# Optimization experiments

Hardware: AMD Instinct MI355X
Metric: run time of the kernel (lower is better)

## Reference

```python
import jax, jax.numpy as jnp
import numpy as np

B, R, F, H, DIM = 256, 64, 2048, 512, 512

def setup_inputs() -> dict:
    key = jax.random.key(0)
    ks = jax.random.split(key, 8)
    s = lambda n: 1.0 / np.sqrt(n)
    return {
        "features": jax.random.normal(ks[0], (B, R, F), jnp.float32),
        "prev": jax.random.normal(ks[1], (B, H), jnp.float32),
        "W_w": jax.random.normal(ks[2], (F, DIM), jnp.float32) * s(F),
        "W_b": jnp.zeros((DIM,), jnp.float32),
        "W2_w": jax.random.normal(ks[3], (H, DIM), jnp.float32) * s(H),
        "W2_b": jnp.zeros((DIM,), jnp.float32),
        "W3_w": jax.random.normal(ks[4], (DIM, 1), jnp.float32) * s(DIM),
        "W3_b": jnp.zeros((1,), jnp.float32),
    }

def reference(features, prev, W_w, W_b, W2_w, W2_b, W3_w, W3_b):
    # prev: [B,H] -> [B,1,DIM]
    p = (prev @ W2_w + W2_b)[:, None, :]
    # features: [B,R,F] -> [B,R,DIM]
    c = jnp.einsum('brf,fd->brd', features, W_w) + W_b
    c = jnp.tanh(c + p)
    score = jnp.einsum('brd,do->bro', c, W3_w) + W3_b  # [B,R,1]
    aw = jax.nn.softmax(score, axis=1)
    q = jnp.sum(aw * features, axis=1)  # [B,F]
    return q
```

## Files before the change

kernel.cpp:

```cpp
#include <hip/hip_runtime.h>
#include <hip/hip_bf16.h>


#define B_ 256
#define R_ 64
#define F_ 2048
#define H_ 512
#define DIM_ 512

typedef short bf16x8 __attribute__((ext_vector_type(8)));
typedef float f32x4 __attribute__((ext_vector_type(4)));

__device__ __forceinline__ ushort f2bf(float x) {
  __hip_bfloat16 h = __float2bfloat16(x);
  return __builtin_bit_cast(ushort, h);
}

__device__ __forceinline__ uint4 pack8(float4 x, float4 y) {
  uint4 r;
  r.x = (uint)f2bf(x.x) | ((uint)f2bf(x.y) << 16);
  r.y = (uint)f2bf(x.z) | ((uint)f2bf(x.w) << 16);
  r.z = (uint)f2bf(y.x) | ((uint)f2bf(y.y) << 16);
  r.w = (uint)f2bf(y.z) | ((uint)f2bf(y.w) << 16);
  return r;
}

__device__ __forceinline__ void gld16(const float* g, float* l) {
  __builtin_amdgcn_global_load_lds(
      (const __attribute__((address_space(1))) unsigned int*)(g),
      (__attribute__((address_space(3))) unsigned int*)(l),
      16, 0, 0);
}

__global__ void pack_w_k(const float* __restrict__ Ww, ushort* __restrict__ wpack) {
  int idx = blockIdx.x * 256 + threadIdx.x;
  float v = Ww[idx];
  int k = idx >> 9;
  int d = idx & 511;
  int kt = k >> 5, kr = k & 31;
  int g = kr >> 3, i = kr & 7;
  int ctg = d >> 4, c = d & 15;
  size_t dst = ((size_t)((kt * 32 + ctg) * 64 + g * 16 + c)) * 8 + (size_t)i;
  wpack[dst] = f2bf(v);
}

__global__ __launch_bounds__(256) void prep_p_k(const float* __restrict__ prev,
                                                const float* __restrict__ W2w,
                                                const float* __restrict__ W2b,
                                                const float* __restrict__ Wb,
                                                float* __restrict__ pprime) {
  __shared__ float lprev[8][H_];
  int bg = blockIdx.x >> 3;
  int d0 = (blockIdx.x & 7) * 64;
  int t = threadIdx.x;
  const float4* src = reinterpret_cast<const float4*>(prev + (size_t)bg * 8 * H_);
  float4* dst = reinterpret_cast<float4*>(&lprev[0][0]);
  for (int i = t; i < 8 * H_ / 4; i += 256) dst[i] = src[i];
  __syncthreads();
  int d = d0 + (t & 63);
  int bq = t >> 6;
  float a0 = 0.f, a1 = 0.f;
  #pragma unroll 8
  for (int h = 0; h < H_; ++h) {
    float wv = W2w[h * DIM_ + d];
    a0 += lprev[bq][h] * wv;
    a1 += lprev[bq + 4][h] * wv;
  }
  float bias = W2b[d] + Wb[d];
  pprime[(size_t)(bg * 8 + bq) * DIM_ + d] = a0 + bias;
  pprime[(size_t)(bg * 8 + bq + 4) * DIM_ + d] = a1 + bias;
}

__device__ __forceinline__ float fast_tanh(float x) {
  float e = __expf(2.f * x);
  return 1.f - 2.f / (e + 1.f);
}

__global__ __launch_bounds__(512, 4) void score_k(const float* __restrict__ feat,
                                                  const ushort* __restrict__ wpack,
                                                  const float* __restrict__ pprime,
                                                  const float* __restrict__ W3,
                                                  float* __restrict__ sp) {
  int slice = blockIdx.x >> 8;
  int b = blockIdx.x & 255;
  int t = threadIdx.x;
  int wid = t >> 6;
  int l = t & 63;
  int l15 = l & 15, g = l >> 4;
  const float* featB = feat + (size_t)b * R_ * F_;

  __shared__ float raw[3][4096];
  __shared__ uint4 frg[2][512];
  __shared__ float lds_part[8][R_];

  f32x4 acc[4][2];
  #pragma unroll
  for (int rt = 0; rt < 4; ++rt)
    #pragma unroll
    for (int ct = 0; ct < 2; ++ct)
      acc[rt][ct] = (f32x4){0.f, 0.f, 0.f, 0.f};

  int srow = wid * 4 + g;
  int sch = l15 ^ (srow & 15);
  const float* sg0 = featB + (size_t)srow * F_ + sch * 4;
  const float* sg1 = featB + (size_t)(srow + 32) * F_ + sch * 4;

  int crow = t >> 3, cj2 = (t & 7) * 2;
  int rm = crow & 15;
  int cw = (t & 7) * 64 + (crow ^ (cj2 & 15));

  const ushort* wp = wpack + (size_t)(slice * 16 + wid * 2) * 512 + (size_t)l * 8;

#define STAGE(buf, kt) do {                                        \
    gld16(sg0 + (size_t)(kt) * 64, &raw[buf][wid * 256]);          \
    gld16(sg1 + (size_t)(kt) * 64, &raw[buf][2048 + wid * 256]);   \
  } while (0)

#define LOADB(dst, kt) do {                                        \
    const ushort* wpk_ = wp + (size_t)(kt) * 32768;                \
    dst[0][0] = *reinterpret_cast<const uint4*>(wpk_);             \
    dst[0][1] = *reinterpret_cast<const uint4*>(wpk_ + 512);       \
    dst[1][0] = *reinterpret_cast<const uint4*>(wpk_ + 16384);     \
    dst[1][1] = *reinterpret_cast<const uint4*>(wpk_ + 16384 + 512); \
  } while (0)

#define CVT(nb, fb) do {                                           \
    const float* rb_ = &raw[nb][crow * 64];                        \
    float4 x_ = *reinterpret_cast<const float4*>(rb_ + ((cj2 + 0) ^ rm) * 4); \
    float4 y_ = *reinterpret_cast<const float4*>(rb_ + ((cj2 + 1) ^ rm) * 4); \
    frg[fb][cw] = pack8(x_, y_);                                   \
  } while (0)

#define MFMA_STEP(fb) do {                                         \
    _Pragma("unroll")                                              \
    for (int s_ = 0; s_ < 2; ++s_) {                               \
      bf16x8 af_[4];                                               \
      int kc_ = s_ * 4 + g;                                        \
      _Pragma("unroll")                                            \
      for (int rt_ = 0; rt_ < 4; ++rt_)                            \
        af_[rt_] = __builtin_bit_cast(bf16x8,                      \
            frg[fb][kc_ * 64 + ((rt_ * 16 + l15) ^ ((kc_ * 2) & 15))]); \
      _Pragma("unroll")                                            \
      for (int ct_ = 0; ct_ < 2; ++ct_) {                          \
        bf16x8 bv_ = __builtin_bit_cast(bf16x8, bc[s_][ct_]);      \
        _Pragma("unroll")                                          \
        for (int rt_ = 0; rt_ < 4; ++rt_)                          \
          acc[rt_][ct_] = __builtin_amdgcn_mfma_f32_16x16x32_bf16( \
              af_[rt_], bv_, acc[rt_][ct_], 0, 0, 0);              \
      }                                                            \
    }                                                              \
  } while (0)

  uint4 bc[2][2];
  STAGE(0, 0);
  STAGE(1, 1);
  LOADB(bc, 0);
  asm volatile("s_waitcnt vmcnt(6)" ::: "memory");
  __builtin_amdgcn_s_barrier();
  asm volatile("" ::: "memory");
  STAGE(2, 2);
  CVT(0, 0);

  int cur3 = 0;
  for (int kt = 0; kt < 32; ++kt) {
    uint4 bn[2][2];
    if (kt < 31) LOADB(bn, kt + 1);
    if (kt < 30) {
      asm volatile("s_waitcnt vmcnt(10) lgkmcnt(0)" ::: "memory");
    } else if (kt == 30) {
      asm volatile("s_waitcnt vmcnt(8) lgkmcnt(0)" ::: "memory");
    } else {
      asm volatile("s_waitcnt lgkmcnt(0)" ::: "memory");
    }
    __builtin_amdgcn_s_barrier();
    asm volatile("" ::: "memory");

    if (kt < 29) STAGE(cur3, kt + 3);
    int nxt3 = (cur3 == 2) ? 0 : cur3 + 1;
    if (kt < 31) CVT(nxt3, (kt + 1) & 1);
    MFMA_STEP(kt & 1);
    if (kt < 31) {
      #pragma unroll
      for (int s_ = 0; s_ < 2; ++s_)
        #pragma unroll
        for (int ct_ = 0; ct_ < 2; ++ct_)
          bc[s_][ct_] = bn[s_][ct_];
    }
    cur3 = nxt3;
  }

#undef STAGE
#undef LOADB
#undef CVT
#undef MFMA_STEP

  float pp[2], w3v[2];
  #pragma unroll
  for (int ct = 0; ct < 2; ++ct) {
    int col = slice * 256 + wid * 32 + ct * 16 + l15;
    pp[ct] = pprime[b * DIM_ + col];
    w3v[ct] = W3[col];
  }
  #pragma unroll
  for (int rt = 0; rt < 4; ++rt) {
    #pragma unroll
    for (int j = 0; j < 4; ++j) {
      float v = fast_tanh(acc[rt][0][j] + pp[0]) * w3v[0]
              + fast_tanh(acc[rt][1][j] + pp[1]) * w3v[1];
      v += __shfl_xor(v, 1);
      v += __shfl_xor(v, 2);
      v += __shfl_xor(v, 4);
      v += __shfl_xor(v, 8);
      if (l15 == 0) lds_part[wid][rt * 16 + g * 4 + j] = v;
    }
  }
  __syncthreads();

  if (t < R_) {
    float s = 0.f;
    #pragma unroll
    for (int w = 0; w < 8; ++w) s += lds_part[w][t];
    sp[((size_t)b * 2 + slice) * R_ + t] = s;
  }
}

__global__ __launch_bounds__(256) void wsum_k(const float* __restrict__ feat,
                                              const float* __restrict__ sp,
                                              float* __restrict__ out) {
  int b = blockIdx.x >> 2;
  int f0 = (blockIdx.x & 3) * 512;
  int t = threadIdx.x;
  __shared__ float lds_aw[R_];

  if (t < R_) {
    float s = sp[((size_t)b * 2 + 0) * R_ + t] + sp[((size_t)b * 2 + 1) * R_ + t];
    float m = s;
    #pragma unroll
    for (int off = 32; off >= 1; off >>= 1) m = fmaxf(m, __shfl_xor(m, off));
    float e = __expf(s - m);
    float su = e;
    #pragma unroll
    for (int off = 32; off >= 1; off >>= 1) su += __shfl_xor(su, off);
    lds_aw[t] = e / su;
  }
  __syncthreads();

  const float* fp = feat + (size_t)b * R_ * F_ + f0 + t * 2;
  float qx = 0.f, qy = 0.f;
  #pragma unroll 8
  for (int r = 0; r < R_; ++r) {
    float a = lds_aw[r];
    float2 v = *reinterpret_cast<const float2*>(fp + (size_t)r * F_);
    qx += a * v.x;
    qy += a * v.y;
  }
  *reinterpret_cast<float2*>(out + (size_t)b * F_ + f0 + t * 2) = (float2){qx, qy};
}

extern "C" void kernel_launch(void* const* d_in, const int* in_sizes, int n_in,
                              void* d_out, int out_size, void* d_ws, size_t ws_size,
                              hipStream_t stream) {
  const float* feat = (const float*)d_in[0];
  const float* prev = (const float*)d_in[1];
  const float* Ww   = (const float*)d_in[2];
  const float* Wb   = (const float*)d_in[3];
  const float* W2w  = (const float*)d_in[4];
  const float* W2b  = (const float*)d_in[5];
  const float* W3w  = (const float*)d_in[6];
  float* out = (float*)d_out;

  ushort* wpack  = (ushort*)d_ws;
  float*  pprime = (float*)((char*)d_ws + (size_t)F_ * DIM_ * 2);
  float*  sp     = (float*)((char*)d_ws + (size_t)F_ * DIM_ * 2
                                        + (size_t)B_ * DIM_ * 4);

  pack_w_k<<<(F_ * DIM_) / 256, 256, 0, stream>>>(Ww, wpack);
  prep_p_k<<<256, 256, 0, stream>>>(prev, W2w, W2b, Wb, pprime);
  score_k<<<B_ * 2, 512, 0, stream>>>(feat, wpack, pprime, W3w, sp);
  wsum_k<<<B_ * 4, 256, 0, stream>>>(feat, sp, out);
}
```

Measured before the change: 103.4 us.

## Enlarge score GEMM tile to 128x256 with 2x4 wave grid and XCD-aware block swizzle

Each score_k block now computes 128 rows (two batch items) by 256 columns instead of 64x256, with waves arranged 2x4 and each wave holding a 64x64 accumulator tile. The larger tile halves the number of packed-weight reads per feature row and cuts the grid to 256 blocks, remapped so neighbouring logical tiles land on the same XCD. The staging ring drops from three buffers to two, and the MFMA phase is wrapped in s_setprio. In exchange, register pressure and LDS use per block go up, occupancy drops to 2 blocks per CU, and the shallower prefetch pipeline may expose more memory latency.

```diff
diff --git a/kernel.cpp b/kernel.cpp
--- a/kernel.cpp
+++ b/kernel.cpp
@@ -76,117 +76,121 @@
   return 1.f - 2.f / (e + 1.f);
 }
 
-__global__ __launch_bounds__(512, 4) void score_k(const float* __restrict__ feat,
+__global__ __launch_bounds__(512, 2) void score_k(const float* __restrict__ feat,
                                                   const ushort* __restrict__ wpack,
                                                   const float* __restrict__ pprime,
                                                   const float* __restrict__ W3,
                                                   float* __restrict__ sp) {
-  int slice = blockIdx.x >> 8;
-  int b = blockIdx.x & 255;
+  int bid = blockIdx.x;
+  int logical = (bid & 7) * 32 + (bid >> 3);
+  int rowblk = logical >> 1;
+  int colblk = logical & 1;
   int t = threadIdx.x;
   int wid = t >> 6;
-  int l = t & 63;
-  int l15 = l & 15, g = l >> 4;
-  const float* featB = feat + (size_t)b * R_ * F_;
-
-  __shared__ float raw[3][4096];
-  __shared__ uint4 frg[2][512];
+  int wm = wid >> 2, wn = wid & 3;
+  int l = t & 63, l15 = l & 15, g = l >> 4;
+
+  const float* featT = feat + (size_t)rowblk * 128 * F_;
+
+  __shared__ float4 raw4[2][2048];
+  __shared__ uint4 frg[2][1024];
   __shared__ float lds_part[8][R_];
 
-  f32x4 acc[4][2];
+  f32x4 acc[4][4];
   #pragma unroll
   for (int rt = 0; rt < 4; ++rt)
     #pragma unroll
-    for (int ct = 0; ct < 2; ++ct)
+    for (int ct = 0; ct < 4; ++ct)
       acc[rt][ct] = (f32x4){0.f, 0.f, 0.f, 0.f};
 
-  int srow = wid * 4 + g;
-  int sch = l15 ^ (srow & 15);
-  const float* sg0 = featB + (size_t)srow * F_ + sch * 4;
-  const float* sg1 = featB + (size_t)(srow + 32) * F_ + sch * 4;
-
-  int crow = t >> 3, cj2 = (t & 7) * 2;
+  const float* sgj[4];
+  #pragma unroll
+  for (int j = 0; j < 4; ++j) {
+    int r_ = wid * 16 + j * 4 + g;
+    int ch = l15 ^ (r_ & 15);
+    sgj[j] = featT + (size_t)r_ * F_ + ch * 4;
+  }
+
+  int crow = t >> 2;
   int rm = crow & 15;
-  int cw = (t & 7) * 64 + (crow ^ (cj2 & 15));
-
-  const ushort* wp = wpack + (size_t)(slice * 16 + wid * 2) * 512 + (size_t)l * 8;
-
-#define STAGE(buf, kt) do {                                        \
-    gld16(sg0 + (size_t)(kt) * 64, &raw[buf][wid * 256]);          \
-    gld16(sg1 + (size_t)(kt) * 64, &raw[buf][2048 + wid * 256]);   \
-  } while (0)
-
-#define LOADB(dst, kt) do {                                        \
-    const ushort* wpk_ = wp + (size_t)(kt) * 32768;                \
-    dst[0][0] = *reinterpret_cast<const uint4*>(wpk_);             \
-    dst[0][1] = *reinterpret_cast<const uint4*>(wpk_ + 512);       \
-    dst[1][0] = *reinterpret_cast<const uint4*>(wpk_ + 16384);     \
-    dst[1][1] = *reinterpret_cast<const uint4*>(wpk_ + 16384 + 512); \
-  } while (0)
-
-#define CVT(nb, fb) do {                                           \
-    const float* rb_ = &raw[nb][crow * 64];                        \
-    float4 x_ = *reinterpret_cast<const float4*>(rb_ + ((cj2 + 0) ^ rm) * 4); \
-    float4 y_ = *reinterpret_cast<const float4*>(rb_ + ((cj2 + 1) ^ rm) * 4); \
-    frg[fb][cw] = pack8(x_, y_);                                   \
-  } while (0)
-
-#define MFMA_STEP(fb) do {                                         \
-    _Pragma("unroll")                                              \
-    for (int s_ = 0; s_ < 2; ++s_) {                               \
-      bf16x8 af_[4];                                               \
-      int kc_ = s_ * 4 + g;                                        \
-      _Pragma("unroll")                                            \
-      for (int rt_ = 0; rt_ < 4; ++rt_)                            \
-        af_[rt_] = __builtin_bit_cast(bf16x8,                      \
-            frg[fb][kc_ * 64 + ((rt_ * 16 + l15) ^ ((kc_ * 2) & 15))]); \
-      _Pragma("unroll")                                            \
-      for (int ct_ = 0; ct_ < 2; ++ct_) {                          \
-        bf16x8 bv_ = __builtin_bit_cast(bf16x8, bc[s_][ct_]);      \
-        _Pragma("unroll")                                          \
-        for (int rt_ = 0; rt_ < 4; ++rt_)                          \
-          acc[rt_][ct_] = __builtin_amdgcn_mfma_f32_16x16x32_bf16( \
-              af_[rt_], bv_, acc[rt_][ct_], 0, 0, 0);              \
-      }                                                            \
-    }                                                              \
-  } while (0)
-
-  uint4 bc[2][2];
+  int cq = (t & 3) * 2;
+
+  int ctg0 = colblk * 16 + wn * 4;
+
+#define STAGE(buf, kt) do {                                          \
+    _Pragma("unroll")                                                \
+    for (int j_ = 0; j_ < 4; ++j_)                                   \
+      gld16(sgj[j_] + (size_t)(kt) * 64,                             \
+            (float*)&raw4[buf][(wid * 16 + j_ * 4) * 16]);           \
+  } while (0)
+
+#define LOADB(dst, kt) do {                                          \
+    _Pragma("unroll")                                                \
+    for (int s_ = 0; s_ < 2; ++s_)                                   \
+      _Pragma("unroll")                                              \
+      for (int ct_ = 0; ct_ < 4; ++ct_)                              \
+        dst[s_][ct_] = *reinterpret_cast<const uint4*>(              \
+            wpack + ((size_t)((kt) * 2 + s_) * 32 + (ctg0 + ct_)) * 512 + (size_t)l * 8); \
+  } while (0)
+
+#define CVT(rb, fb) do {                                             \
+    _Pragma("unroll")                                                \
+    for (int h_ = 0; h_ < 2; ++h_) {                                 \
+      int kc_ = cq + h_;                                             \
+      float4 x_ = raw4[rb][crow * 16 + ((kc_ * 2) ^ rm)];            \
+      float4 y_ = raw4[rb][crow * 16 + ((kc_ * 2 + 1) ^ rm)];        \
+      frg[fb][kc_ * 128 + crow] = pack8(x_, y_);                     \
+    }                                                                \
+  } while (0)
+
+#define MFMA_STEP(fb) do {                                           \
+    _Pragma("unroll")                                                \
+    for (int s_ = 0; s_ < 2; ++s_) {                                 \
+      bf16x8 af_[4];                                                 \
+      _Pragma("unroll")                                              \
+      for (int rt_ = 0; rt_ < 4; ++rt_)                              \
+        af_[rt_] = __builtin_bit_cast(bf16x8,                        \
+            frg[fb][(s_ * 4 + g) * 128 + wm * 64 + rt_ * 16 + l15]); \
+      _Pragma("unroll")                                              \
+      for (int ct_ = 0; ct_ < 4; ++ct_) {                            \
+        bf16x8 bv_ = __builtin_bit_cast(bf16x8, bc[s_][ct_]);        \
+        _Pragma("unroll")                                            \
+        for (int rt_ = 0; rt_ < 4; ++rt_)                            \
+          acc[rt_][ct_] = __builtin_amdgcn_mfma_f32_16x16x32_bf16(   \
+              af_[rt_], bv_, acc[rt_][ct_], 0, 0, 0);                \
+      }                                                              \
+    }                                                                \
+  } while (0)
+
+  uint4 bc[2][4], bn[2][4];
   STAGE(0, 0);
   STAGE(1, 1);
   LOADB(bc, 0);
-  asm volatile("s_waitcnt vmcnt(6)" ::: "memory");
-  __builtin_amdgcn_s_barrier();
-  asm volatile("" ::: "memory");
-  STAGE(2, 2);
+  asm volatile("s_waitcnt vmcnt(12)" ::: "memory");
   CVT(0, 0);
 
-  int cur3 = 0;
   for (int kt = 0; kt < 32; ++kt) {
-    uint4 bn[2][2];
     if (kt < 31) LOADB(bn, kt + 1);
-    if (kt < 30) {
-      asm volatile("s_waitcnt vmcnt(10) lgkmcnt(0)" ::: "memory");
-    } else if (kt == 30) {
+    if (kt < 31) {
       asm volatile("s_waitcnt vmcnt(8) lgkmcnt(0)" ::: "memory");
     } else {
-      asm volatile("s_waitcnt lgkmcnt(0)" ::: "memory");
+      asm volatile("s_waitcnt vmcnt(0) lgkmcnt(0)" ::: "memory");
     }
     __builtin_amdgcn_s_barrier();
     asm volatile("" ::: "memory");
 
-    if (kt < 29) STAGE(cur3, kt + 3);
-    int nxt3 = (cur3 == 2) ? 0 : cur3 + 1;
-    if (kt < 31) CVT(nxt3, (kt + 1) & 1);
+    if (kt < 30) STAGE(kt & 1, kt + 2);
+    if (kt < 31) CVT((kt + 1) & 1, (kt + 1) & 1);
+    __builtin_amdgcn_s_setprio(1);
     MFMA_STEP(kt & 1);
+    __builtin_amdgcn_s_setprio(0);
     if (kt < 31) {
       #pragma unroll
       for (int s_ = 0; s_ < 2; ++s_)
         #pragma unroll
-        for (int ct_ = 0; ct_ < 2; ++ct_)
+        for (int ct_ = 0; ct_ < 4; ++ct_)
           bc[s_][ct_] = bn[s_][ct_];
     }
-    cur3 = nxt3;
   }
 
 #undef STAGE
@@ -194,11 +198,12 @@
 #undef CVT
 #undef MFMA_STEP
 
-  float pp[2], w3v[2];
-  #pragma unroll
-  for (int ct = 0; ct < 2; ++ct) {
-    int col = slice * 256 + wid * 32 + ct * 16 + l15;
-    pp[ct] = pprime[b * DIM_ + col];
+  int b0 = rowblk * 2;
+  float pp[4], w3v[4];
+  #pragma unroll
+  for (int ct = 0; ct < 4; ++ct) {
+    int col = colblk * 256 + wn * 64 + ct * 16 + l15;
+    pp[ct] = pprime[(b0 + wm) * DIM_ + col];
     w3v[ct] = W3[col];
   }
   #pragma unroll
@@ -206,7 +211,9 @@
     #pragma unroll
     for (int j = 0; j < 4; ++j) {
       float v = fast_tanh(acc[rt][0][j] + pp[0]) * w3v[0]
-              + fast_tanh(acc[rt][1][j] + pp[1]) * w3v[1];
+              + fast_tanh(acc[rt][1][j] + pp[1]) * w3v[1]
+              + fast_tanh(acc[rt][2][j] + pp[2]) * w3v[2]
+              + fast_tanh(acc[rt][3][j] + pp[3]) * w3v[3];
       v += __shfl_xor(v, 1);
       v += __shfl_xor(v, 2);
       v += __shfl_xor(v, 4);
@@ -216,11 +223,12 @@
   }
   __syncthreads();
 
-  if (t < R_) {
-    float s = 0.f;
-    #pragma unroll
-    for (int w = 0; w < 8; ++w) s += lds_part[w][t];
-    sp[((size_t)b * 2 + slice) * R_ + t] = s;
+  if (t < 128) {
+    int bb = t >> 6;
+    int r = t & 63;
+    float s = lds_part[bb * 4 + 0][r] + lds_part[bb * 4 + 1][r]
+            + lds_part[bb * 4 + 2][r] + lds_part[bb * 4 + 3][r];
+    sp[((size_t)(b0 + bb) * 2 + colblk) * R_ + r] = s;
   }
 }
 
@@ -276,6 +284,6 @@
 
   pack_w_k<<<(F_ * DIM_) / 256, 256, 0, stream>>>(Ww, wpack);
   prep_p_k<<<256, 256, 0, stream>>>(prev, W2w, W2b, Wb, pprime);
-  score_k<<<B_ * 2, 512, 0, stream>>>(feat, wpack, pprime, W3w, sp);
+  score_k<<<256, 512, 0, stream>>>(feat, wpack, pprime, W3w, sp);
   wsum_k<<<B_ * 4, 256, 0, stream>>>(feat, sp, out);
 }
```

Result: slower. 113.2 us (+9.5%).

## Merge setup kernels and unroll score k-loop with double B registers and setprio

Applied to the files above, without the earlier changes.

Merges the weight-packing and prev-projection kernels into one launch, with a block-index split, to save one kernel launch. The score kernel's k-loop is unrolled by two and uses two ping-pong B-fragment register sets instead of copying the next fragments each iteration. MFMA sections are wrapped in s_setprio to favour the math waves. The triple-buffer indices are tracked explicitly, and the final iterations are peeled with adjusted waitcnts. Register pressure and code size grow.

```diff
diff --git a/kernel.cpp b/kernel.cpp
--- a/kernel.cpp
+++ b/kernel.cpp
@@ -32,26 +32,29 @@
       16, 0, 0);
 }
 
-__global__ void pack_w_k(const float* __restrict__ Ww, ushort* __restrict__ wpack) {
-  int idx = blockIdx.x * 256 + threadIdx.x;
-  float v = Ww[idx];
-  int k = idx >> 9;
-  int d = idx & 511;
-  int kt = k >> 5, kr = k & 31;
-  int g = kr >> 3, i = kr & 7;
-  int ctg = d >> 4, c = d & 15;
-  size_t dst = ((size_t)((kt * 32 + ctg) * 64 + g * 16 + c)) * 8 + (size_t)i;
-  wpack[dst] = f2bf(v);
-}
-
-__global__ __launch_bounds__(256) void prep_p_k(const float* __restrict__ prev,
-                                                const float* __restrict__ W2w,
-                                                const float* __restrict__ W2b,
-                                                const float* __restrict__ Wb,
-                                                float* __restrict__ pprime) {
+__global__ __launch_bounds__(256) void setup_k(const float* __restrict__ Ww,
+                                               ushort* __restrict__ wpack,
+                                               const float* __restrict__ prev,
+                                               const float* __restrict__ W2w,
+                                               const float* __restrict__ W2b,
+                                               const float* __restrict__ Wb,
+                                               float* __restrict__ pprime) {
   __shared__ float lprev[8][H_];
-  int bg = blockIdx.x >> 3;
-  int d0 = (blockIdx.x & 7) * 64;
+  if (blockIdx.x < 4096) {
+    int idx = blockIdx.x * 256 + threadIdx.x;
+    float v = Ww[idx];
+    int k = idx >> 9;
+    int d = idx & 511;
+    int kt = k >> 5, kr = k & 31;
+    int g = kr >> 3, i = kr & 7;
+    int ctg = d >> 4, c = d & 15;
+    size_t dst = ((size_t)((kt * 32 + ctg) * 64 + g * 16 + c)) * 8 + (size_t)i;
+    wpack[dst] = f2bf(v);
+    return;
+  }
+  int pb = blockIdx.x - 4096;
+  int bg = pb >> 3;
+  int d0 = (pb & 7) * 64;
   int t = threadIdx.x;
   const float4* src = reinterpret_cast<const float4*>(prev + (size_t)bg * 8 * H_);
   float4* dst = reinterpret_cast<float4*>(&lprev[0][0]);
@@ -107,7 +110,7 @@
 
   int crow = t >> 3, cj2 = (t & 7) * 2;
   int rm = crow & 15;
-  int cw = (t & 7) * 64 + (crow ^ (cj2 & 15));
+  int cw = (t & 7) * 64 + (crow ^ cj2);
 
   const ushort* wp = wpack + (size_t)(slice * 16 + wid * 2) * 512 + (size_t)l * 8;
 
@@ -131,7 +134,7 @@
     frg[fb][cw] = pack8(x_, y_);                                   \
   } while (0)
 
-#define MFMA_STEP(fb) do {                                         \
+#define MFMA_STEP(fb, BSET) do {                                   \
     _Pragma("unroll")                                              \
     for (int s_ = 0; s_ < 2; ++s_) {                               \
       bf16x8 af_[4];                                               \
@@ -142,7 +145,7 @@
             frg[fb][kc_ * 64 + ((rt_ * 16 + l15) ^ ((kc_ * 2) & 15))]); \
       _Pragma("unroll")                                            \
       for (int ct_ = 0; ct_ < 2; ++ct_) {                          \
-        bf16x8 bv_ = __builtin_bit_cast(bf16x8, bc[s_][ct_]);      \
+        bf16x8 bv_ = __builtin_bit_cast(bf16x8, BSET[s_][ct_]);    \
         _Pragma("unroll")                                          \
         for (int rt_ = 0; rt_ < 4; ++rt_)                          \
           acc[rt_][ct_] = __builtin_amdgcn_mfma_f32_16x16x32_bf16( \
@@ -151,48 +154,72 @@
     }                                                              \
   } while (0)
 
-  uint4 bc[2][2];
+#define BARRIER_VM(N) do {                                         \
+    asm volatile("s_waitcnt vmcnt(" #N ") lgkmcnt(0)" ::: "memory"); \
+    __builtin_amdgcn_s_barrier();                                  \
+    asm volatile("" ::: "memory");                                 \
+  } while (0)
+
+  uint4 bA[2][2], bB[2][2];
   STAGE(0, 0);
   STAGE(1, 1);
-  LOADB(bc, 0);
+  LOADB(bA, 0);
   asm volatile("s_waitcnt vmcnt(6)" ::: "memory");
   __builtin_amdgcn_s_barrier();
   asm volatile("" ::: "memory");
   STAGE(2, 2);
   CVT(0, 0);
 
-  int cur3 = 0;
-  for (int kt = 0; kt < 32; ++kt) {
-    uint4 bn[2][2];
-    if (kt < 31) LOADB(bn, kt + 1);
-    if (kt < 30) {
-      asm volatile("s_waitcnt vmcnt(10) lgkmcnt(0)" ::: "memory");
-    } else if (kt == 30) {
-      asm volatile("s_waitcnt vmcnt(8) lgkmcnt(0)" ::: "memory");
-    } else {
-      asm volatile("s_waitcnt lgkmcnt(0)" ::: "memory");
-    }
-    __builtin_amdgcn_s_barrier();
-    asm volatile("" ::: "memory");
-
-    if (kt < 29) STAGE(cur3, kt + 3);
-    int nxt3 = (cur3 == 2) ? 0 : cur3 + 1;
-    if (kt < 31) CVT(nxt3, (kt + 1) & 1);
-    MFMA_STEP(kt & 1);
-    if (kt < 31) {
-      #pragma unroll
-      for (int s_ = 0; s_ < 2; ++s_)
-        #pragma unroll
-        for (int ct_ = 0; ct_ < 2; ++ct_)
-          bc[s_][ct_] = bn[s_][ct_];
-    }
-    cur3 = nxt3;
-  }
+  int st_b = 0, cv_b = 1;
+  for (int e = 0; e < 28; e += 2) {
+    LOADB(bB, e + 1);
+    BARRIER_VM(10);
+    STAGE(st_b, e + 3);
+    CVT(cv_b, 1);
+    __builtin_amdgcn_s_setprio(1);
+    MFMA_STEP(0, bA);
+    __builtin_amdgcn_s_setprio(0);
+    st_b = (st_b == 2) ? 0 : st_b + 1;
+    cv_b = (cv_b == 2) ? 0 : cv_b + 1;
+    LOADB(bA, e + 2);
+    BARRIER_VM(10);
+    STAGE(st_b, e + 4);
+    CVT(cv_b, 0);
+    __builtin_amdgcn_s_setprio(1);
+    MFMA_STEP(1, bB);
+    __builtin_amdgcn_s_setprio(0);
+    st_b = (st_b == 2) ? 0 : st_b + 1;
+    cv_b = (cv_b == 2) ? 0 : cv_b + 1;
+  }
+  LOADB(bB, 29);
+  BARRIER_VM(10);
+  STAGE(1, 31);
+  CVT(2, 1);
+  __builtin_amdgcn_s_setprio(1);
+  MFMA_STEP(0, bA);
+  __builtin_amdgcn_s_setprio(0);
+  LOADB(bA, 30);
+  BARRIER_VM(10);
+  CVT(0, 0);
+  __builtin_amdgcn_s_setprio(1);
+  MFMA_STEP(1, bB);
+  __builtin_amdgcn_s_setprio(0);
+  LOADB(bB, 31);
+  BARRIER_VM(8);
+  CVT(1, 1);
+  __builtin_amdgcn_s_setprio(1);
+  MFMA_STEP(0, bA);
+  __builtin_amdgcn_s_setprio(0);
+  BARRIER_VM(0);
+  __builtin_amdgcn_s_setprio(1);
+  MFMA_STEP(1, bB);
+  __builtin_amdgcn_s_setprio(0);
 
 #undef STAGE
 #undef LOADB
 #undef CVT
 #undef MFMA_STEP
+#undef BARRIER_VM
 
   float pp[2], w3v[2];
   #pragma unroll
@@ -274,8 +301,7 @@
   float*  sp     = (float*)((char*)d_ws + (size_t)F_ * DIM_ * 2
                                         + (size_t)B_ * DIM_ * 4);
 
-  pack_w_k<<<(F_ * DIM_) / 256, 256, 0, stream>>>(Ww, wpack);
-  prep_p_k<<<256, 256, 0, stream>>>(prev, W2w, W2b, Wb, pprime);
+  setup_k<<<4096 + 256, 256, 0, stream>>>(Ww, wpack, prev, W2w, W2b, Wb, pprime);
   score_k<<<B_ * 2, 512, 0, stream>>>(feat, wpack, pprime, W3w, sp);
   wsum_k<<<B_ * 4, 256, 0, stream>>>(feat, sp, out);
 }
```

Result: faster. 98.37 us (-4.9%).
